# Kernel optimization log

Hardware: AMD Instinct MI355X
Metric: run time of the kernel (lower is better)

## Reference

```python
import jax, jax.numpy as jnp
import numpy as np
from jax.scipy.special import logsumexp


def setup_inputs() -> dict:
    key = jax.random.key(0)
    B, C, H, W = 2, 32, 128, 128
    sizes = [(H, W)] + [(H // 2, W // 2)] * 4
    ks = iter(jax.random.split(key, 32))
    inp = {}
    for t, (hh, ww) in enumerate(sizes):
        inp[f"unary_h{t}"] = jax.random.normal(next(ks), (B, C, hh, ww), jnp.float32)
        inp[f"unary_v{t}"] = jax.random.normal(next(ks), (B, C, hh, ww), jnp.float32)
        inp[f"pairwise_h{t}"] = 0.1 * jax.random.normal(next(ks), (B, C, C, hh, ww - 1), jnp.float32)
        inp[f"pairwise_v{t}"] = 0.1 * jax.random.normal(next(ks), (B, C, C, hh - 1, ww), jnp.float32)
    inp["gamma"] = jnp.ones((1,), jnp.float32)
    return inp


def _chain_marginals(unary, pairwise, gamma):
    """Entropy-smoothed max-product marginals along the LAST axis.
    unary: [B,C,L,T], pairwise: [B,C,C,L,T-1] (pairwise[b,i,j,l,t] couples state i at t with j at t+1).
    Returns soft marginals [B,C,L,T] (softmax over C per position)."""
    u = jnp.transpose(unary, (3, 0, 2, 1))        # [T,B,L,C]
    pw = jnp.transpose(pairwise, (4, 0, 3, 1, 2))  # [T-1,B,L,C,C]
    inv_g = 1.0 / gamma

    def fwd_step(f, xs):
        u_t, pw_t = xs
        f_new = u_t + gamma * logsumexp(f[..., :, None] * inv_g + pw_t * inv_g, axis=-2)
        return f_new, f_new

    _, f_rest = jax.lax.scan(fwd_step, u[0], (u[1:], pw))
    f = jnp.concatenate([u[:1], f_rest], axis=0)

    def bwd_step(bb, xs):
        u_t, pw_t = xs
        b_new = u_t + gamma * logsumexp(bb[..., None, :] * inv_g + pw_t * inv_g, axis=-1)
        return b_new, b_new

    _, b_rest = jax.lax.scan(bwd_step, u[-1], (u[:-1][::-1], pw[::-1]))
    b = jnp.concatenate([u[-1:], b_rest], axis=0)[::-1]

    marg = jax.nn.softmax((f + b - u) * inv_g, axis=-1)  # [T,B,L,C]
    return jnp.transpose(marg, (1, 3, 2, 0))             # [B,C,L,T]


def _dp_pair(uh, uv, ph, pv, g):
    # horizontal chains (along W) with unary_h, vertical chains (along H) with unary_v
    mh = _chain_marginals(uh, ph, g)
    mv = _chain_marginals(uv.swapaxes(2, 3), pv.swapaxes(3, 4), g).swapaxes(2, 3)
    return mh, mv


def _scatter_up(m, stride, i, j, H, W):
    # max_unpool2d with the structured indices: m[y,x] -> (i + y*stride, j + x*stride), then crop/pad to (H,W)
    b, c, h_, w_ = m.shape
    up = jnp.zeros((b, c, h_ * stride, w_ * stride), m.dtype).at[:, :, i::stride, j::stride].set(m)
    up = up[:, :, :H, :W]
    ph, pw = H - up.shape[2], W - up.shape[3]
    if ph > 0 or pw > 0:
        up = jnp.pad(up, ((0, 0), (0, 0), (0, max(ph, 0)), (0, max(pw, 0))))
    return up


def reference(unary_h0, unary_h1, unary_h2, unary_h3, unary_h4,
              unary_v0, unary_v1, unary_v2, unary_v3, unary_v4,
              pairwise_h0, pairwise_h1, pairwise_h2, pairwise_h3, pairwise_h4,
              pairwise_v0, pairwise_v1, pairwise_v2, pairwise_v3, pairwise_v4,
              gamma):
    uh = [unary_h0, unary_h1, unary_h2, unary_h3, unary_h4]
    uv = [unary_v0, unary_v1, unary_v2, unary_v3, unary_v4]
    ph = [pairwise_h0, pairwise_h1, pairwise_h2, pairwise_h3, pairwise_h4]
    pv = [pairwise_v0, pairwise_v1, pairwise_v2, pairwise_v3, pairwise_v4]
    g = jnp.clip(gamma.reshape(()), 0.01)  # learned gamma, clamped min 0.01

    H, W = uh[0].shape[2], uh[0].shape[3]
    alpha = 1.0 / W if W > H else 1.0 / H

    mh0, mv0 = _dp_pair(uh[0], uv[0], ph[0], pv[0], g)
    marg_hs, marg_vs = [mh0], [mv0]
    mh_acc, mv_acc = mh0, mv0

    stride, cnt = 2, 1  # step_size = 1 default -> one extra scale with a 2x2 shifted grid
    for i in range(stride):
        for j in range(stride):
            m_h, m_v = _dp_pair(uh[cnt], uv[cnt], ph[cnt], pv[cnt], g)
            marg_hs.append(m_h)
            marg_vs.append(m_v)
            mh_acc = mh_acc + _scatter_up(m_h, stride, i, j, H, W)
            mv_acc = mv_acc + _scatter_up(m_v, stride, i, j, H, W)
            cnt += 1

    num_pairwise_terms = 2
    avg = (mh_acc + mv_acc) / (num_pairwise_terms * 2)

    new_uh0 = uh[0] - alpha * (marg_hs[0] - avg)
    new_uv0 = uv[0] - alpha * (marg_vs[0] - avg)
    # fine-scale unary updates (computed for faithfulness; gradients flow through avg)
    cnt = 1
    new_uh_fine, new_uv_fine = [], []
    for i in range(stride):
        for j in range(stride):
            new_uh_fine.append(uh[cnt] - alpha * (marg_hs[cnt] - avg[:, :, i::stride, j::stride]))
            new_uv_fine.append(uv[cnt] - alpha * (marg_vs[cnt] - avg[:, :, i::stride, j::stride]))
            cnt += 1

    main = jnp.stack([new_uh0, new_uv0, mh_acc, mv_acc], axis=0)  # [4,B,C,H,W]
    return main
```

## Files before the change

### kernel.cpp

```cpp
#include <hip/hip_runtime.h>
#include <stdint.h>

#define TC 2
#define CHUNK_BYTES 4096
#define CHUNK_F4 256

static __device__ __forceinline__ float softmax32_l2(float z)
{
  float zm = z;
  zm = fmaxf(zm, __shfl_xor(zm, 16));
  zm = fmaxf(zm, __shfl_xor(zm, 8));
  zm = fmaxf(zm, __shfl_xor(zm, 4));
  zm = fmaxf(zm, __shfl_xor(zm, 2));
  zm = fmaxf(zm, __shfl_xor(zm, 1));
  float p = exp2f(z - zm);
  float ps = p;
  ps += __shfl_xor(ps, 16);
  ps += __shfl_xor(ps, 8);
  ps += __shfl_xor(ps, 4);
  ps += __shfl_xor(ps, 2);
  ps += __shfl_xor(ps, 1);
  return p / ps;
}

static __device__ __forceinline__ uint32_t pkbf(float a, float b)
{
  uint32_t ua = __float_as_uint(a), ub = __float_as_uint(b);
  ua = (ua + 0x7FFFu + ((ua >> 16) & 1u)) >> 16;
  ub = (ub + 0x7FFFu + ((ub >> 16) & 1u)) & 0xFFFF0000u;
  return ua | ub;
}

static __device__ __forceinline__ float rfl(float x)
{
  return __int_as_float(__builtin_amdgcn_readfirstlane(__float_as_int(x)));
}

#define RLF(x, i) __int_as_float(__builtin_amdgcn_readlane(__float_as_int(x), (i)))

static __device__ __forceinline__ float dot16_rl(const float* w, float e, int h)
{
  float a0, a1, a2, a3, b0, b1, b2, b3;
  a0 = w[0]  * RLF(e, 0)  + w[1]  * RLF(e, 1);
  a1 = w[2]  * RLF(e, 2)  + w[3]  * RLF(e, 3);
  a2 = w[4]  * RLF(e, 4)  + w[5]  * RLF(e, 5);
  a3 = w[6]  * RLF(e, 6)  + w[7]  * RLF(e, 7);
  a0 += w[8]  * RLF(e, 8)  + w[9]  * RLF(e, 9);
  a1 += w[10] * RLF(e, 10) + w[11] * RLF(e, 11);
  a2 += w[12] * RLF(e, 12) + w[13] * RLF(e, 13);
  a3 += w[14] * RLF(e, 14) + w[15] * RLF(e, 15);
  float dlo = (a0 + a1) + (a2 + a3);
  b0 = w[0]  * RLF(e, 16) + w[1]  * RLF(e, 17);
  b1 = w[2]  * RLF(e, 18) + w[3]  * RLF(e, 19);
  b2 = w[4]  * RLF(e, 20) + w[5]  * RLF(e, 21);
  b3 = w[6]  * RLF(e, 22) + w[7]  * RLF(e, 23);
  b0 += w[8]  * RLF(e, 24) + w[9]  * RLF(e, 25);
  b1 += w[10] * RLF(e, 26) + w[11] * RLF(e, 27);
  b2 += w[12] * RLF(e, 28) + w[13] * RLF(e, 29);
  b3 += w[14] * RLF(e, 30) + w[15] * RLF(e, 31);
  float dhi = (b0 + b1) + (b2 + b3);
  return h ? dhi : dlo;
}

struct TSeg { const float* pw; uint16_t* PT; int L, Tt, Tpad, fStride, Xtot, dirV, blockBase, nx, ny; };
struct TTable { TSeg s[10]; int nseg; };
struct USeg { const float* U; float* Ut; int fs, nx, ny, L, T, dirV, blockBase; };
struct UTable { USeg s[10]; int nseg; };
struct DSeg { const uint16_t* PT; const float* Ut; float* F; float* B; int chainBase, T, Tt, Tpad; };
struct DTable { DSeg s[10]; int nseg; };
struct MSeg { const float* F; const float* B; const float* Ut; float* out; int L, T, dirV, blockBase, nrx, nfx; };
struct MTable { MSeg s[10]; int nseg; };

__global__ __launch_bounds__(256) void k_transpose_all(TTable tbl, const float* __restrict__ gamma)
{
  __shared__ uint16_t tile[128][128];
  int bid = blockIdx.x;
  int k = 0;
  for (int q = 1; q < tbl.nseg; q++) if (bid >= tbl.s[q].blockBase) k = q;
  TSeg sg = tbl.s[k];
  float igl2 = 1.4426950408889634f / fmaxf(gamma[0], 0.01f);
  int r = bid - sg.blockBase;
  int jg = r & 7; r >>= 3;
  int w = r % sg.nx; int tmp = r / sg.nx;
  int fixed = tmp % sg.ny;
  int b = tmp / sg.ny;
  int j0 = jg * 4;
  int g = fixed * sg.fStride;
  int a = g & 31;
  int xbase = w * 128 - a;
  if (xbase >= sg.Xtot) return;
  int tid = threadIdx.x;
  int kx = tid & 31, psub = tid >> 5;
  int pstride = sg.L * sg.Tt;
  int clampMax = 2048 * pstride - 4;
  int jthr = j0 + (psub & 3);
  int swj = (jthr >> 1) & 3;
  int gp0 = ((psub >> 2) << 5) + jthr;
  int idx0 = ((b << 10) + gp0) * pstride + (g - a) + (w << 7) + (kx << 2);
  const float* pw = sg.pw;
  #pragma unroll
  for (int hp = 0; hp < 2; hp++) {
    float4 st[8];
    #pragma unroll
    for (int q = 0; q < 8; q++) {
      int batch = hp * 8 + q;
      int idx = idx0 + batch * (pstride << 6);
      idx = idx > clampMax ? clampMax : idx;
      st[q] = *(const float4*)(pw + idx);
    }
    #pragma unroll
    for (int q = 0; q < 8; q++) {
      int batch = hp * 8 + q;
      int i = 2 * batch + (psub >> 2);
      int sw = swj ^ (((i >> 3) & 3) << 2);
      int pl = batch * 8 + psub;
      uint32_t pk0 = pkbf(exp2f(st[q].x * igl2), exp2f(st[q].y * igl2));
      uint32_t pk1 = pkbf(exp2f(st[q].z * igl2), exp2f(st[q].w * igl2));
      if (sw & 1) { uint32_t tswp = pk0; pk0 = pk1; pk1 = tswp; }
      *(uint2*)((unsigned char*)tile + pl * 256 + 8 * (kx ^ (sw >> 1))) = make_uint2(pk0, pk1);
    }
  }
  __syncthreads();
  uint32_t* PTd = (uint32_t*)sg.PT;
  #pragma unroll
  for (int w8 = 0; w8 < 8; w8++) {
    int gidx = w8 * 256 + tid;
    int xs = gidx >> 4;
    int q = gidx & 15;
    int xv = xbase + xs;
    if (xv < 0 || xv >= sg.Xtot) continue;
    int jl = q >> 2, j = j0 + jl;
    int perm3 = (j >> 1) & 7;
    int swjW = (j >> 1) & 3;
    uint32_t pk[4];
    #pragma unroll
    for (int e = 0; e < 4; e++) {
      int wd = ((q & 3) << 2) + e;
      int pos = wd >> 1, pr = wd & 1;
      int i0 = ((pos ^ perm3) << 2) + pr * 2;
      int sw = swjW ^ (((i0 >> 3) & 3) << 2);
      int c = (xs >> 1) ^ sw;
      int u16c = (c << 1) | (xs & 1);
      int r0 = (i0 << 2) + jl;
      uint32_t v0 = tile[r0][u16c];
      uint32_t v1 = tile[r0 + 4][u16c];
      pk[e] = v0 | (v1 << 16);
    }
    int chain, tsl;
    if (sg.dirV) { chain = b * sg.Xtot + xv; tsl = fixed; }
    else         { chain = b * sg.ny + fixed; tsl = xv; }
    *(uint4*)&PTd[((size_t)chain * sg.Tpad + tsl) * 512 + j * 16 + (q & 3) * 4] =
        make_uint4(pk[0], pk[1], pk[2], pk[3]);
  }
}

__global__ __launch_bounds__(256) void k_ut_all(UTable tbl, const float* __restrict__ gamma)
{
  __shared__ float tile[32][33];
  int bid = blockIdx.x;
  int k = 0;
  for (int q = 1; q < tbl.nseg; q++) if (bid >= tbl.s[q].blockBase) k = q;
  USeg sg = tbl.s[k];
  float igl2 = 1.4426950408889634f / fmaxf(gamma[0], 0.01f);
  int r = bid - sg.blockBase;
  int bx = r % sg.nx; int tmp = r / sg.nx;
  int fixed = tmp % sg.ny;
  int b = tmp / sg.ny;
  int tid = threadIdx.x;
  size_t LT = (size_t)sg.L * sg.T;
  int x0 = bx * 32;
  int xx = tid & 31;
  #pragma unroll
  for (int it = 0; it < 4; it++) {
    int c = (tid >> 5) + it * 8;
    tile[xx][c] = sg.U[(size_t)b * 32 * LT + (size_t)c * LT + (size_t)fixed * sg.fs + x0 + xx];
  }
  __syncthreads();
  int xw = tid >> 3;
  int ci = (tid & 7) * 4;
  int chain = sg.dirV ? b * sg.L + x0 + xw : b * sg.L + fixed;
  int tIdx  = sg.dirV ? fixed : x0 + xw;
  float4 vv = make_float4(tile[xw][ci] * igl2, tile[xw][ci + 1] * igl2,
                          tile[xw][ci + 2] * igl2, tile[xw][ci + 3] * igl2);
  *(float4*)&sg.Ut[((size_t)chain * sg.T + tIdx) * 32 + ci] = vv;
}

__global__ __launch_bounds__(256) void k_dp_all(DTable tbl, int nDP)
{
  __shared__ __align__(16) unsigned char ldsAll[4][2 * CHUNK_BYTES + 1024];
  int wid = threadIdx.x >> 6;
  unsigned char* lds = ldsAll[wid];
  float* f_out = (float*)(lds + 2 * CHUNK_BYTES);
  int gw = blockIdx.x * 4 + wid;
  if (gw >= 2 * nDP) return;
  int isB = (gw >= nDP) ? 1 : 0;
  int bid = gw - isB * nDP;
  int k = 0;
  for (int q = 1; q < tbl.nseg; q++) if (bid >= tbl.s[q].chainBase) k = q;
  DSeg sg = tbl.s[k];
  int chain = bid - sg.chainBase;
  int T = sg.T, Tt = sg.Tt;
  int tid = threadIdx.x & 63, j = tid & 31, h = tid >> 5;
  const float* Utc = sg.Ut + (size_t)chain * T * 32;
  float* Oc = (isB ? sg.B : sg.F) + (size_t)chain * T * 32;
  const float4* src = (const float4*)(sg.PT + (size_t)chain * sg.Tpad * 1024);
  int nch = sg.Tpad / TC;
  int perm3 = (j >> 1) & 7;
  float4 stg[4];
  float uCur[TC], uNxt[TC];
  if (!isB) {
    float cur = Utc[j];
    if (h == 0) f_out[j] = cur;
    float eCur = exp2f(cur - rfl(cur));
    #pragma unroll
    for (int ss = 0; ss < TC; ss++) {
      int t = ss + 1; t = t > Tt ? Tt : t;
      uCur[ss] = Utc[(size_t)t * 32 + j];
    }
    #pragma unroll
    for (int q = 0; q < 4; q++) stg[q] = src[q * 64 + tid];
    int buf = 0;
    for (int ch = 0; ch < nch; ch++) {
      float4* dst = (float4*)(lds + buf * CHUNK_BYTES);
      #pragma unroll
      for (int q = 0; q < 4; q++) dst[q * 64 + tid] = stg[q];
      if (ch + 1 < nch) {
        const float4* s2 = src + (size_t)(ch + 1) * CHUNK_F4;
        #pragma unroll
        for (int q = 0; q < 4; q++) stg[q] = s2[q * 64 + tid];
        #pragma unroll
        for (int ss = 0; ss < TC; ss++) {
          int t = (ch + 1) * TC + ss + 1; t = t > Tt ? Tt : t;
          uNxt[ss] = Utc[(size_t)t * 32 + j];
        }
      }
      #pragma unroll
      for (int ss = 0; ss < TC; ss++) {
        int s = ch * TC + ss;
        if (s >= Tt) break;
        int t = s + 1;
        const uint32_t* sl = (const uint32_t*)(lds + buf * CHUNK_BYTES + ss * 2048);
        float w[16];
        #pragma unroll
        for (int rr = 0; rr < 4; rr++) {
          int pos = (4 * h + rr) ^ perm3;
          uint2 dv = *(const uint2*)&sl[j * 16 + pos * 2];
          w[rr * 4 + 0] = __uint_as_float(dv.x << 16);
          w[rr * 4 + 1] = __uint_as_float(dv.x & 0xFFFF0000u);
          w[rr * 4 + 2] = __uint_as_float(dv.y << 16);
          w[rr * 4 + 3] = __uint_as_float(dv.y & 0xFFFF0000u);
        }
        float dot = dot16_rl(w, eCur, h);
        float dot2 = dot + __shfl_xor(dot, 32);
        cur = uCur[ss] + __log2f(dot2);
        if (h == 0) f_out[(t & 7) * 32 + j] = cur;
        eCur = exp2f(cur - rfl(cur));
        if ((t & 7) == 7) {
          float4 vv = *(float4*)&f_out[tid * 4];
          *(float4*)&Oc[(size_t)(t - 7) * 32 + tid * 4] = vv;
        }
      }
      #pragma unroll
      for (int ss = 0; ss < TC; ss++) uCur[ss] = uNxt[ss];
      buf ^= 1;
    }
  } else {
    int p2i = j >> 2, pri = (j >> 1) & 1, loi = j & 1;
    float cur = Utc[(size_t)(T - 1) * 32 + j];
    if (h == 0) f_out[7 * 32 + j] = cur;
    float eCur = exp2f(cur - rfl(cur));
    #pragma unroll
    for (int ss = 0; ss < TC; ss++) {
      int s = (nch - 1) * TC + ss; s = s > Tt - 1 ? Tt - 1 : s; s = s < 0 ? 0 : s;
      uCur[ss] = Utc[(size_t)s * 32 + j];
    }
    {
      const float4* s2 = src + (size_t)(nch - 1) * CHUNK_F4;
      #pragma unroll
      for (int q = 0; q < 4; q++) stg[q] = s2[q * 64 + tid];
    }
    int buf = 0;
    for (int ch = nch - 1; ch >= 0; ch--) {
      float4* dst = (float4*)(lds + buf * CHUNK_BYTES);
      #pragma unroll
      for (int q = 0; q < 4; q++) dst[q * 64 + tid] = stg[q];
      if (ch > 0) {
        const float4* s2 = src + (size_t)(ch - 1) * CHUNK_F4;
        #pragma unroll
        for (int q = 0; q < 4; q++) stg[q] = s2[q * 64 + tid];
        #pragma unroll
        for (int ss = 0; ss < TC; ss++) {
          int s = (ch - 1) * TC + ss; s = s > Tt - 1 ? Tt - 1 : s; s = s < 0 ? 0 : s;
          uNxt[ss] = Utc[(size_t)s * 32 + j];
        }
      }
      #pragma unroll
      for (int ss = TC - 1; ss >= 0; ss--) {
        int s = ch * TC + ss;
        if (s >= Tt) continue;
        const uint16_t* row16 = (const uint16_t*)(lds + buf * CHUNK_BYTES + ss * 2048);
        float w[16];
        #pragma unroll
        for (int jj = 0; jj < 16; jj++) {
          int u16idx = (16 * h + jj) * 32 + ((p2i ^ (jj >> 1)) * 2 + pri) * 2 + loi;
          w[jj] = __uint_as_float((uint32_t)row16[u16idx] << 16);
        }
        float dot = dot16_rl(w, eCur, h);
        float dot2 = dot + __shfl_xor(dot, 32);
        cur = uCur[ss] + __log2f(dot2);
        if (h == 0) f_out[(s & 7) * 32 + j] = cur;
        eCur = exp2f(cur - rfl(cur));
        if ((s & 7) == 0) {
          float4 vv = *(float4*)&f_out[tid * 4];
          *(float4*)&Oc[(size_t)s * 32 + tid * 4] = vv;
        }
      }
      #pragma unroll
      for (int ss = 0; ss < TC; ss++) uCur[ss] = uNxt[ss];
      buf ^= 1;
    }
  }
}

__global__ __launch_bounds__(256) void k_marg_all(MTable tbl)
{
  __shared__ float sm[32][33];
  int bid = blockIdx.x;
  int k = 0;
  for (int q = 1; q < tbl.nseg; q++) if (bid >= tbl.s[q].blockBase) k = q;
  MSeg sg = tbl.s[k];
  int r = bid - sg.blockBase;
  int rx = r % sg.nrx; int tmp = r / sg.nrx;
  int fx = tmp % sg.nfx; int b = tmp / sg.nfx;
  int tid = threadIdx.x;
  int c = tid & 31;
  int L = sg.L, T = sg.T;
  size_t LT = (size_t)L * T;
  int RA = sg.dirV ? L : T;
  int r0 = rx * 32;
  #pragma unroll
  for (int pass = 0; pass < 4; pass++) {
    int rr = (tid >> 5) + pass * 8;
    int rowAxis = r0 + rr;
    int chain = sg.dirV ? b * L + rowAxis : b * L + fx;
    int t = sg.dirV ? fx : rowAxis;
    size_t idx = ((size_t)chain * T + t) * 32 + c;
    float z = sg.F[idx] + sg.B[idx] - sg.Ut[idx];
    sm[rr][c] = softmax32_l2(z);
  }
  __syncthreads();
  int cc = tid >> 3;
  int xl = (tid & 7) * 4;
  size_t obase = (size_t)b * 32 * LT + (size_t)fx * RA + r0;
  float4 vv = make_float4(sm[xl][cc], sm[xl + 1][cc], sm[xl + 2][cc], sm[xl + 3][cc]);
  *(float4*)&sg.out[obase + (size_t)cc * LT + xl] = vv;
}

__global__ __launch_bounds__(256) void k_combine(
    const float* __restrict__ uh0, const float* __restrict__ uv0,
    const float* __restrict__ MB, float* __restrict__ out)
{
  int t4 = blockIdx.x * 256 + threadIdx.x;
  int base = t4 * 4;
  int x = base & 127, y = (base >> 7) & 127;
  int bc = base >> 14;
  float4 mh0 = *(const float4*)&MB[base];
  float4 mv0 = *(const float4*)&MB[1048576 + base];
  int ce = 1 + ((y & 1) << 1);
  int coff = bc * 4096 + ((y >> 1) << 6) + (x >> 1);
  const float* cbE = MB + 2097152 + (size_t)(ce - 1) * 524288;
  const float* cbO = cbE + 524288;
  float2 mhcE = *(const float2*)&cbE[coff];
  float2 mhcO = *(const float2*)&cbO[coff];
  float2 mvcE = *(const float2*)&cbE[262144 + coff];
  float2 mvcO = *(const float2*)&cbO[262144 + coff];
  float4 u_h = *(const float4*)&uh0[base];
  float4 u_v = *(const float4*)&uv0[base];
  float mh[4] = {mh0.x, mh0.y, mh0.z, mh0.w};
  float mv[4] = {mv0.x, mv0.y, mv0.z, mv0.w};
  float uh[4] = {u_h.x, u_h.y, u_h.z, u_h.w};
  float uv[4] = {u_v.x, u_v.y, u_v.z, u_v.w};
  float mhc[4] = {mhcE.x, mhcO.x, mhcE.y, mhcO.y};
  float mvc[4] = {mvcE.x, mvcO.x, mvcE.y, mvcO.y};
  float o0[4], o1[4], o2[4], o3[4];
  const float A = 0.0078125f;
  #pragma unroll
  for (int e = 0; e < 4; e++) {
    float mha = mh[e] + mhc[e], mva = mv[e] + mvc[e];
    float avg = (mha + mva) * 0.25f;
    o0[e] = uh[e] - A * (mh[e] - avg);
    o1[e] = uv[e] - A * (mv[e] - avg);
    o2[e] = mha; o3[e] = mva;
  }
  *(float4*)&out[base]           = make_float4(o0[0], o0[1], o0[2], o0[3]);
  *(float4*)&out[1048576 + base] = make_float4(o1[0], o1[1], o1[2], o1[3]);
  *(float4*)&out[2097152 + base] = make_float4(o2[0], o2[1], o2[2], o2[3]);
  *(float4*)&out[3145728 + base] = make_float4(o3[0], o3[1], o3[2], o3[3]);
}

static void fill_tseg(TSeg& t, const float* pw, uint16_t* PT, int L, int T, int dirV, int blockBase)
{
  int Tt = T - 1;
  t.pw = pw; t.PT = PT;
  t.L = L; t.Tt = Tt; t.Tpad = T;
  t.fStride = dirV ? L : Tt;
  t.Xtot = dirV ? L : Tt;
  t.dirV = dirV;
  int pad = (t.fStride & 31) ? 31 : 0;
  t.nx = (t.Xtot + pad + 127) / 128;
  t.ny = dirV ? Tt : L;
  t.blockBase = blockBase;
}

extern "C" void kernel_launch(void* const* d_in, const int* in_sizes, int n_in,
                              void* d_out, int out_size, void* d_ws, size_t ws_size,
                              hipStream_t stream)
{
  (void)in_sizes; (void)n_in; (void)out_size;
  const float* gamma = (const float*)d_in[20];
  unsigned char* ws = (unsigned char*)d_ws;

  int segL[10], segT[10];
  const float* segPW[10]; const float* segUU[10];
  size_t segMG[10];
  for (int lvl = 0; lvl < 5; lvl++) {
    int H = lvl ? 64 : 128, W = H;
    int si = lvl * 2;
    segL[si] = H; segT[si] = W;
    segPW[si] = (const float*)d_in[lvl * 4 + 2];
    segUU[si] = (const float*)d_in[lvl * 4 + 0];
    segL[si + 1] = W; segT[si + 1] = H;
    segPW[si + 1] = (const float*)d_in[lvl * 4 + 3];
    segUU[si + 1] = (const float*)d_in[lvl * 4 + 1];
    if (lvl == 0) { segMG[0] = 0; segMG[1] = 1048576; }
    else { segMG[si] = 2097152 + (size_t)(lvl - 1) * 524288; segMG[si + 1] = segMG[si] + 262144; }
  }

  const size_t NEED = 318767104ull;
  if (ws_size >= NEED) {
    uint16_t* PT0 = (uint16_t*)ws;
    float* MARG = (float*)ws;
    float* F0  = (float*)(ws + 268435456ull);
    float* B0  = (float*)(ws + 285212672ull);
    float* Ut0 = (float*)(ws + 301989888ull);

    TTable tt; UTable ut; DTable dt; MTable mt;
    tt.nseg = 10; ut.nseg = 10; dt.nseg = 10; mt.nseg = 10;
    size_t ptOff = 0, fuOff = 0;
    int tB = 0, uB = 0, cB = 0, mB = 0;
    for (int s = 0; s < 10; s++) {
      int dirV = s & 1;
      int L = segL[s], T = segT[s];
      int chains = 2 * L;
      fill_tseg(tt.s[s], segPW[s], PT0 + ptOff, L, T, dirV, tB);
      tB += 2 * tt.s[s].ny * tt.s[s].nx * 8;
      USeg& u = ut.s[s];
      u.U = segUU[s]; u.Ut = Ut0 + fuOff;
      u.fs = dirV ? L : T;
      u.nx = (dirV ? L : T) / 32;
      u.ny = dirV ? T : L;
      u.L = L; u.T = T; u.dirV = dirV;
      u.blockBase = uB;
      uB += u.nx * u.ny * 2;
      DSeg& d = dt.s[s];
      d.PT = PT0 + ptOff; d.Ut = Ut0 + fuOff;
      d.F = F0 + fuOff; d.B = B0 + fuOff;
      d.chainBase = cB; d.T = T; d.Tt = T - 1; d.Tpad = T;
      cB += chains;
      MSeg& m = mt.s[s];
      m.F = F0 + fuOff; m.B = B0 + fuOff; m.Ut = Ut0 + fuOff;
      m.out = MARG + segMG[s];
      m.L = L; m.T = T; m.dirV = dirV;
      m.blockBase = mB;
      m.nrx = (dirV ? L : T) / 32;
      m.nfx = dirV ? T : L;
      mB += 2 * m.nfx * m.nrx;
      ptOff += (size_t)chains * T * 1024;
      fuOff += (size_t)chains * T * 32;
    }
    k_transpose_all<<<tB, 256, 0, stream>>>(tt, gamma);
    k_ut_all<<<uB, 256, 0, stream>>>(ut, gamma);
    k_dp_all<<<(2 * cB + 3) / 4, 256, 0, stream>>>(dt, cB);
    k_marg_all<<<mB, 256, 0, stream>>>(mt);
    k_combine<<<1024, 256, 0, stream>>>((const float*)d_in[0], (const float*)d_in[1],
                                        MARG, (float*)d_out);
  } else {
    uint16_t* PT0 = (uint16_t*)ws;
    float* F0  = (float*)(ws + 67108864ull);
    float* B0  = (float*)(ws + 71303168ull);
    float* Ut0 = (float*)(ws + 75497472ull);
    float* MARG = (float*)(ws + 79691776ull);
    for (int s = 0; s < 10; s++) {
      int dirV = s & 1;
      int L = segL[s], T = segT[s];
      int chains = 2 * L;
      TTable tt; tt.nseg = 1;
      fill_tseg(tt.s[0], segPW[s], PT0, L, T, dirV, 0);
      int nb = 2 * tt.s[0].ny * tt.s[0].nx * 8;
      k_transpose_all<<<nb, 256, 0, stream>>>(tt, gamma);
      UTable ut; ut.nseg = 1;
      USeg& u = ut.s[0];
      u.U = segUU[s]; u.Ut = Ut0;
      u.fs = dirV ? L : T;
      u.nx = (dirV ? L : T) / 32;
      u.ny = dirV ? T : L;
      u.L = L; u.T = T; u.dirV = dirV; u.blockBase = 0;
      int ub = u.nx * u.ny * 2;
      k_ut_all<<<ub, 256, 0, stream>>>(ut, gamma);
      DTable dt; dt.nseg = 1;
      DSeg& d = dt.s[0];
      d.PT = PT0; d.Ut = Ut0; d.F = F0; d.B = B0;
      d.chainBase = 0; d.T = T; d.Tt = T - 1; d.Tpad = T;
      k_dp_all<<<(2 * chains + 3) / 4, 256, 0, stream>>>(dt, chains);
      MTable mt; mt.nseg = 1;
      MSeg& m = mt.s[0];
      m.F = F0; m.B = B0; m.Ut = Ut0; m.out = MARG + segMG[s];
      m.L = L; m.T = T; m.dirV = dirV; m.blockBase = 0;
      m.nrx = (dirV ? L : T) / 32;
      m.nfx = dirV ? T : L;
      int mb = 2 * m.nfx * m.nrx;
      k_marg_all<<<mb, 256, 0, stream>>>(mt);
    }
    k_combine<<<1024, 256, 0, stream>>>((const float*)d_in[0], (const float*)d_in[1],
                                        MARG, (float*)d_out);
  }
}
```

Baseline: 385.8 us.

## Split transpose+DP into two phases to reuse PT buffer in cache; nontemporal pw loads

Splits the transposed-pairwise build and the DP pass into two phases: segments 0-1 (full-resolution level), then segments 2-9 (the half-resolution levels). Each phase writes its PT buffer starting at offset zero, so the DP kernel reads it back while it is more likely to still be in cache. Pairwise inputs are loaded with nontemporal hints so this streaming-once data does not evict other cached lines. The cost is two extra kernel launches and less parallelism within each launch.

```diff
diff --git a/kernel.cpp b/kernel.cpp
--- a/kernel.cpp
+++ b/kernel.cpp
@@ -4,6 +4,8 @@
 #define TC 2
 #define CHUNK_BYTES 4096
 #define CHUNK_F4 256
+
+typedef float floatx4 __attribute__((ext_vector_type(4)));
 
 static __device__ __forceinline__ float softmax32_l2(float z)
 {
@@ -100,13 +102,13 @@
   const float* pw = sg.pw;
   #pragma unroll
   for (int hp = 0; hp < 2; hp++) {
-    float4 st[8];
+    floatx4 st[8];
     #pragma unroll
     for (int q = 0; q < 8; q++) {
       int batch = hp * 8 + q;
       int idx = idx0 + batch * (pstride << 6);
       idx = idx > clampMax ? clampMax : idx;
-      st[q] = *(const float4*)(pw + idx);
+      st[q] = __builtin_nontemporal_load((const floatx4*)(pw + idx));
     }
     #pragma unroll
     for (int q = 0; q < 8; q++) {
@@ -444,43 +446,68 @@
     float* B0  = (float*)(ws + 285212672ull);
     float* Ut0 = (float*)(ws + 301989888ull);
 
-    TTable tt; UTable ut; DTable dt; MTable mt;
-    tt.nseg = 10; ut.nseg = 10; dt.nseg = 10; mt.nseg = 10;
-    size_t ptOff = 0, fuOff = 0;
-    int tB = 0, uB = 0, cB = 0, mB = 0;
+    size_t fuOffOf[10];
+    {
+      size_t fuOff = 0;
+      for (int s = 0; s < 10; s++) {
+        fuOffOf[s] = fuOff;
+        fuOff += (size_t)(2 * segL[s]) * segT[s] * 32;
+      }
+    }
+
+    UTable ut; ut.nseg = 10;
+    int uB = 0;
     for (int s = 0; s < 10; s++) {
       int dirV = s & 1;
-      int L = segL[s], T = segT[s];
-      int chains = 2 * L;
-      fill_tseg(tt.s[s], segPW[s], PT0 + ptOff, L, T, dirV, tB);
-      tB += 2 * tt.s[s].ny * tt.s[s].nx * 8;
       USeg& u = ut.s[s];
-      u.U = segUU[s]; u.Ut = Ut0 + fuOff;
-      u.fs = dirV ? L : T;
-      u.nx = (dirV ? L : T) / 32;
-      u.ny = dirV ? T : L;
-      u.L = L; u.T = T; u.dirV = dirV;
+      u.U = segUU[s]; u.Ut = Ut0 + fuOffOf[s];
+      u.fs = dirV ? segL[s] : segT[s];
+      u.nx = (dirV ? segL[s] : segT[s]) / 32;
+      u.ny = dirV ? segT[s] : segL[s];
+      u.L = segL[s]; u.T = segT[s]; u.dirV = dirV;
       u.blockBase = uB;
       uB += u.nx * u.ny * 2;
-      DSeg& d = dt.s[s];
-      d.PT = PT0 + ptOff; d.Ut = Ut0 + fuOff;
-      d.F = F0 + fuOff; d.B = B0 + fuOff;
-      d.chainBase = cB; d.T = T; d.Tt = T - 1; d.Tpad = T;
-      cB += chains;
+    }
+    k_ut_all<<<uB, 256, 0, stream>>>(ut, gamma);
+
+    const int phEnd[3] = {0, 2, 10};
+    for (int ph = 0; ph < 2; ph++) {
+      TTable tt; DTable dt;
+      int s0 = phEnd[ph], s1 = phEnd[ph + 1];
+      tt.nseg = s1 - s0; dt.nseg = s1 - s0;
+      size_t ptOff = 0;
+      int tB = 0, cB = 0;
+      for (int s = s0; s < s1; s++) {
+        int i = s - s0;
+        int dirV = s & 1;
+        int L = segL[s], T = segT[s];
+        int chains = 2 * L;
+        fill_tseg(tt.s[i], segPW[s], PT0 + ptOff, L, T, dirV, tB);
+        tB += 2 * tt.s[i].ny * tt.s[i].nx * 8;
+        DSeg& d = dt.s[i];
+        d.PT = PT0 + ptOff; d.Ut = Ut0 + fuOffOf[s];
+        d.F = F0 + fuOffOf[s]; d.B = B0 + fuOffOf[s];
+        d.chainBase = cB; d.T = T; d.Tt = T - 1; d.Tpad = T;
+        cB += chains;
+        ptOff += (size_t)chains * T * 1024;
+      }
+      k_transpose_all<<<tB, 256, 0, stream>>>(tt, gamma);
+      k_dp_all<<<(2 * cB + 3) / 4, 256, 0, stream>>>(dt, cB);
+    }
+
+    MTable mt; mt.nseg = 10;
+    int mB = 0;
+    for (int s = 0; s < 10; s++) {
+      int dirV = s & 1;
       MSeg& m = mt.s[s];
-      m.F = F0 + fuOff; m.B = B0 + fuOff; m.Ut = Ut0 + fuOff;
+      m.F = F0 + fuOffOf[s]; m.B = B0 + fuOffOf[s]; m.Ut = Ut0 + fuOffOf[s];
       m.out = MARG + segMG[s];
-      m.L = L; m.T = T; m.dirV = dirV;
+      m.L = segL[s]; m.T = segT[s]; m.dirV = dirV;
       m.blockBase = mB;
-      m.nrx = (dirV ? L : T) / 32;
-      m.nfx = dirV ? T : L;
+      m.nrx = (dirV ? segL[s] : segT[s]) / 32;
+      m.nfx = dirV ? segT[s] : segL[s];
       mB += 2 * m.nfx * m.nrx;
-      ptOff += (size_t)chains * T * 1024;
-      fuOff += (size_t)chains * T * 32;
-    }
-    k_transpose_all<<<tB, 256, 0, stream>>>(tt, gamma);
-    k_ut_all<<<uB, 256, 0, stream>>>(ut, gamma);
-    k_dp_all<<<(2 * cB + 3) / 4, 256, 0, stream>>>(dt, cB);
+    }
     k_marg_all<<<mB, 256, 0, stream>>>(mt);
     k_combine<<<1024, 256, 0, stream>>>((const float*)d_in[0], (const float*)d_in[1],
                                         MARG, (float*)d_out);
```

New measurement: 367.7 us. 4.7% less time.
